# Performance work log

Measured on AMD Instinct MI355X. Metric: run time of the kernel, lower is better.

The kernel has to match this reference:

```python
import jax, jax.numpy as jnp
import numpy as np

B, Q, C = 2, 1568, 768
H = 12
FN, S = 8, 196


def setup_inputs() -> dict:
    key = jax.random.key(0)
    ks = jax.random.split(key, 8)
    init = lambda k, shape: jax.random.normal(k, shape, jnp.float32) * 0.02
    return {
        "query": jax.random.normal(ks[0], (B, Q, C), jnp.float32),
        "memory": jax.random.normal(ks[1], (B, FN * S, C), jnp.float32),
        "Wq": init(ks[2], (C, C)),
        "Wkv": init(ks[3], (C, 2 * C)),
        "Wpq": init(ks[4], (C, C)),
        "Wpkv": init(ks[5], (C, 2 * C)),
        "Wproj": init(ks[6], (C, C)),
        "bproj": jnp.zeros((C,), jnp.float32),
        "seq_len": S,
        "num_frames": FN,
    }


def reference(query, memory, Wq, Wkv, Wpq, Wpkv, Wproj, bproj, seq_len, num_frames):
    Bn, N, Cn = memory.shape
    h = H
    d = Cn // h
    Fn, Sn = num_frames, seq_len
    Qn = query.shape[1]
    scale = d ** -0.5

    # stage 1: per-frame spatial attention
    q = query @ Wq                                   # [B,Q,C]
    k, v = jnp.split(memory @ Wkv, 2, axis=-1)       # [B,N,C] each
    qh = q.reshape(Bn, Qn, h, d)
    kh = k.reshape(Bn, Fn, Sn, h, d)
    vh = v.reshape(Bn, Fn, Sn, h, d)
    space_attn = scale * jnp.einsum('bqhd,bfshd->bhqfs', qh, kh)  # [B,h,Q,F,S]
    attn = jax.nn.softmax(space_attn, axis=-1)        # softmax over tokens within each frame
    # per-frame summaries: [B,Q,F,C]
    x = jnp.einsum('bhqfs,bfshd->bqfhd', attn, vh).reshape(Bn, Qn, Fn, Cn)

    # stage 2: temporal attention over frame summaries
    k2, v2 = jnp.split(x @ Wpkv, 2, axis=-1)
    k2 = k2.reshape(Bn, Qn, Fn, h, d).transpose(0, 3, 1, 2, 4)   # [B,h,Q,F,d]
    v2 = v2.reshape(Bn, Qn, Fn, h, d).transpose(0, 3, 1, 2, 4)   # [B,h,Q,F,d]
    q2 = (q @ Wpq).reshape(Bn, Qn, h, d).transpose(0, 2, 1, 3) * scale  # [B,h,Q,d]
    attn2 = jax.nn.softmax(jnp.einsum('bhqd,bhqfd->bhqf', q2, k2), axis=-1)
    # faithful to source einsum 'b h q f, b h s f d -> b h q d': v2's query axis is summed out
    q_out = jnp.einsum('bhqf,bhsfd->bhqd', attn2, v2)             # [B,h,Q,d]
    q_out = q_out.transpose(0, 2, 1, 3).reshape(Bn, Qn, Cn) @ Wproj + bproj

    # source returns pre-softmax scaled scores with shape (B*h, Q, F, S)
    return q_out, space_attn.reshape(Bn * h, Qn, Fn, Sn)
```

## Files before the change

kernel.cpp:

```cpp
#include <hip/hip_runtime.h>

#define B_   2
#define Q_   1568
#define C_   768
#define C2_  1536
#define H_   12
#define D_   64
#define F_   8
#define S_   196
#define N_   1568
constexpr float SCALE = 0.125f;

typedef __bf16 bf16_t;
typedef __bf16 bf16x8 __attribute__((ext_vector_type(8)));
typedef __bf16 bf16x4 __attribute__((ext_vector_type(4)));
typedef float  f32x4  __attribute__((ext_vector_type(4)));

#define AS_G __attribute__((address_space(1)))
#define AS_L __attribute__((address_space(3)))

__device__ inline void load_lds16(const void* g, void* l) {
    __builtin_amdgcn_global_load_lds((const AS_G unsigned int*)g,
                                     (AS_L unsigned int*)l, 16, 0, 0);
}

__global__ __launch_bounds__(256) void cvt_bf16(
    const float* __restrict__ in, bf16_t* __restrict__ out, int n4)
{
    int i = blockIdx.x * 256 + threadIdx.x;
    if (i < n4) {
        float4 v = ((const float4*)in)[i];
        bf16x4 o = { (bf16_t)v.x, (bf16_t)v.y, (bf16_t)v.z, (bf16_t)v.w };
        ((bf16x4*)out)[i] = o;
    }
}

__global__ __launch_bounds__(256) void transpose_cvt(
    const float* __restrict__ W, bf16_t* __restrict__ Wt, int K, int N)
{
    __shared__ float tile[32][33];
    const int k0 = blockIdx.y * 32, n0 = blockIdx.x * 32;
    const int t = threadIdx.x;
    const int tx = t & 31, ty = t >> 5;
#pragma unroll
    for (int i = 0; i < 4; i++)
        tile[ty + i * 8][tx] = W[(size_t)(k0 + ty + i * 8) * N + n0 + tx];
    __syncthreads();
#pragma unroll
    for (int i = 0; i < 4; i++)
        Wt[(size_t)(n0 + ty + i * 8) * K + k0 + tx] = (bf16_t)tile[tx][ty + i * 8];
}

__global__ __launch_bounds__(256) void gemm_mfma(
    const bf16_t* __restrict__ A, const bf16_t* __restrict__ Bt,
    float* __restrict__ C, bf16_t* __restrict__ Cbf,
    int M, int N, int K, const float* __restrict__ bias)
{
    __shared__ bf16_t As[2][128 * 32];
    __shared__ bf16_t Bs[2][128 * 32];
    const int n0 = blockIdx.x * 128;
    const int m0 = blockIdx.y * 128;
    const int t = threadIdx.x;
    const int lane = t & 63;
    const int wv = t >> 6;
    const int wm = wv >> 1, wn = wv & 1;
    const int lane15 = lane & 15, quad = lane >> 4;

    f32x4 acc[4][4];
#pragma unroll
    for (int i = 0; i < 4; i++)
#pragma unroll
        for (int j = 0; j < 4; j++) acc[i][j] = (f32x4){0.f, 0.f, 0.f, 0.f};

    const int row0 = t >> 2,          kc0 = t & 3;
    const int row1 = (256 + t) >> 2,  kc1 = t & 3;
    int rg0 = m0 + row0; if (rg0 >= M) rg0 = M - 1;
    int rg1 = m0 + row1; if (rg1 >= M) rg1 = M - 1;
    const bf16_t* a0 = A  + (size_t)rg0 * K + kc0 * 8;
    const bf16_t* a1 = A  + (size_t)rg1 * K + kc1 * 8;
    const bf16_t* b0 = Bt + (size_t)(n0 + row0) * K + kc0 * 8;
    const bf16_t* b1 = Bt + (size_t)(n0 + row1) * K + kc1 * 8;
    const int dst0 = (0 * 256 + wv * 64) * 16;
    const int dst1 = (1 * 256 + wv * 64) * 16;

    auto stage = [&](int buf, int k0) {
        load_lds16(a0 + k0, (char*)As[buf] + dst0);
        load_lds16(b0 + k0, (char*)Bs[buf] + dst0);
        load_lds16(a1 + k0, (char*)As[buf] + dst1);
        load_lds16(b1 + k0, (char*)Bs[buf] + dst1);
    };

    stage(0, 0);
    __syncthreads();
    int cur = 0;
    for (int k0 = 0; k0 < K; k0 += 32) {
        if (k0 + 32 < K) stage(cur ^ 1, k0 + 32);

        const bf16_t* Ab = As[cur];
        const bf16_t* Bb = Bs[cur];
        bf16x8 af[4], bfr[4];
#pragma unroll
        for (int i = 0; i < 4; i++) {
            af[i]  = *(const bf16x8*)(Ab + (wm * 64 + i * 16 + lane15) * 32 + quad * 8);
            bfr[i] = *(const bf16x8*)(Bb + (wn * 64 + i * 16 + lane15) * 32 + quad * 8);
        }
#pragma unroll
        for (int i = 0; i < 4; i++)
#pragma unroll
            for (int j = 0; j < 4; j++)
                acc[i][j] = __builtin_amdgcn_mfma_f32_16x16x32_bf16(af[i], bfr[j], acc[i][j], 0, 0, 0);

        __syncthreads();
        cur ^= 1;
    }

#pragma unroll
    for (int i = 0; i < 4; i++) {
#pragma unroll
        for (int j = 0; j < 4; j++) {
            int col = n0 + wn * 64 + j * 16 + lane15;
            float bb = bias ? bias[col] : 0.f;
#pragma unroll
            for (int r = 0; r < 4; r++) {
                int row = m0 + wm * 64 + i * 16 + quad * 4 + r;
                if (row < M) {
                    float v = acc[i][j][r] + bb;
                    if (C)   C[(size_t)row * N + col] = v;
                    if (Cbf) Cbf[(size_t)row * N + col] = (bf16_t)v;
                }
            }
        }
    }
}

__global__ __launch_bounds__(448, 4) void attn1_fused(
    const bf16_t* __restrict__ qb, const bf16_t* __restrict__ kvb,
    float* __restrict__ out1, bf16_t* __restrict__ x, float* __restrict__ xsum)
{
    __shared__ bf16_t Vt[64 * 232];
    __shared__ bf16_t Ps[7 * 16 * 232];
    const int f = blockIdx.x, qt = blockIdx.y, z = blockIdx.z;
    const int b = z / H_, h = z - b * H_;
    const int t = threadIdx.x;
    const int lane = t & 63, w = t >> 6;
    const int lane15 = lane & 15, quad = lane >> 4;

    const size_t kvBase = ((size_t)b * N_ + (size_t)f * S_) * C2_;

    const int qrow = qt * 112 + w * 16 + lane15;
    const bf16_t* qp = qb + ((size_t)b * Q_ + qrow) * C_ + h * D_ + quad * 8;
    bf16x8 qa0 = *(const bf16x8*)(qp);
    bf16x8 qa1 = *(const bf16x8*)(qp + 32);

#pragma unroll
    for (int i = 0; i < 4; i++) {
        int e = t + 448 * i;
        if (e < 64 * 28) {
            int dd = e / 28;
            int s  = S_ + (e - dd * 28);
            Vt[dd * 232 + s] = (bf16_t)0.f;
        }
    }
#pragma unroll
    for (int i = 0; i < 4; i++) {
        int e = t + 448 * i;
        if (e < 8 * S_) {
            int dg = e / S_, s = e - dg * S_;
            bf16x8 v = *(const bf16x8*)(kvb + kvBase + (size_t)s * C2_ + C_ + h * D_ + dg * 8);
#pragma unroll
            for (int j = 0; j < 8; j++)
                Vt[(dg * 8 + j) * 232 + s] = v[j];
        }
    }
    bf16_t* Pw = Ps + w * (16 * 232);
    {
        int prow = lane >> 2, c0 = 208 + (lane & 3) * 4;
        *(bf16x4*)(Pw + prow * 232 + c0) =
            (bf16x4){(bf16_t)0.f, (bf16_t)0.f, (bf16_t)0.f, (bf16_t)0.f};
    }
    __syncthreads();

    f32x4 acc[13];
#pragma unroll
    for (int n = 0; n < 13; n++) acc[n] = (f32x4){0.f, 0.f, 0.f, 0.f};
#pragma unroll
    for (int n = 0; n < 13; n++) {
        int srow = n * 16 + lane15; if (srow > S_ - 1) srow = S_ - 1;
        const bf16_t* kp = kvb + kvBase + (size_t)srow * C2_ + h * D_ + quad * 8;
        bf16x8 kb0 = *(const bf16x8*)(kp);
        bf16x8 kb1 = *(const bf16x8*)(kp + 32);
        acc[n] = __builtin_amdgcn_mfma_f32_16x16x32_bf16(qa0, kb0, acc[n], 0, 0, 0);
        acc[n] = __builtin_amdgcn_mfma_f32_16x16x32_bf16(qa1, kb1, acc[n], 0, 0, 0);
    }

    const size_t o1base = ((size_t)z * Q_ + qt * 112 + w * 16 + quad * 4) * N_ + (size_t)f * S_;
#pragma unroll
    for (int n = 0; n < 13; n++) {
        int s = n * 16 + lane15;
        bool valid = s < S_;
#pragma unroll
        for (int r = 0; r < 4; r++) {
            float v = SCALE * acc[n][r];
            if (valid) out1[o1base + (size_t)r * N_ + s] = v;
            acc[n][r] = valid ? v : -3e38f;
        }
    }

    float m[4], inv[4];
#pragma unroll
    for (int r = 0; r < 4; r++) {
        float mm = acc[0][r];
#pragma unroll
        for (int n = 1; n < 13; n++) mm = fmaxf(mm, acc[n][r]);
        mm = fmaxf(mm, __shfl_xor(mm, 1));
        mm = fmaxf(mm, __shfl_xor(mm, 2));
        mm = fmaxf(mm, __shfl_xor(mm, 4));
        mm = fmaxf(mm, __shfl_xor(mm, 8));
        m[r] = mm;
    }
#pragma unroll
    for (int r = 0; r < 4; r++) {
        float ss = 0.f;
#pragma unroll
        for (int n = 0; n < 13; n++) {
            float e = __expf(acc[n][r] - m[r]);
            acc[n][r] = e;
            ss += e;
        }
        ss += __shfl_xor(ss, 1);
        ss += __shfl_xor(ss, 2);
        ss += __shfl_xor(ss, 4);
        ss += __shfl_xor(ss, 8);
        inv[r] = 1.f / ss;
    }

#pragma unroll
    for (int n = 0; n < 13; n++)
#pragma unroll
        for (int r = 0; r < 4; r++)
            Pw[(quad * 4 + r) * 232 + n * 16 + lane15] = (bf16_t)(acc[n][r] * inv[r]);

    bf16x8 pa[7];
#pragma unroll
    for (int ks = 0; ks < 7; ks++)
        pa[ks] = *(const bf16x8*)(Pw + lane15 * 232 + ks * 32 + quad * 8);

    f32x4 o[4];
#pragma unroll
    for (int nt = 0; nt < 4; nt++) o[nt] = (f32x4){0.f, 0.f, 0.f, 0.f};
#pragma unroll
    for (int nt = 0; nt < 4; nt++)
#pragma unroll
        for (int ks = 0; ks < 7; ks++) {
            bf16x8 vb = *(const bf16x8*)(Vt + (nt * 16 + lane15) * 232 + ks * 32 + quad * 8);
            o[nt] = __builtin_amdgcn_mfma_f32_16x16x32_bf16(pa[ks], vb, o[nt], 0, 0, 0);
        }

    const int qb2 = qt * 112 + w * 16 + quad * 4;
#pragma unroll
    for (int nt = 0; nt < 4; nt++)
#pragma unroll
        for (int r = 0; r < 4; r++)
            x[(((size_t)(b * Q_ + qb2 + r)) * F_ + f) * C_ + h * D_ + nt * 16 + lane15] =
                (bf16_t)o[nt][r];

    float part[4];
#pragma unroll
    for (int nt = 0; nt < 4; nt++)
        part[nt] = o[nt][0] + o[nt][1] + o[nt][2] + o[nt][3];
    __syncthreads();
    float* red = (float*)Vt;
    if (t < 64) red[t] = 0.f;
    __syncthreads();
#pragma unroll
    for (int nt = 0; nt < 4; nt++)
        atomicAdd(&red[nt * 16 + lane15], part[nt]);
    __syncthreads();
    if (t < 64)
        atomicAdd(&xsum[((size_t)(b * F_ + f)) * C_ + h * D_ + t], red[t]);
}

__global__ __launch_bounds__(256) void vsum_kernel(
    const float* __restrict__ xsum, const float* __restrict__ Wpkv,
    float* __restrict__ vsum)
{
    __shared__ float xs[C_];
    const int bf = blockIdx.x;
    const int t = threadIdx.x;
    for (int i = 0; i < 3; i++) xs[t + 256 * i] = xsum[(size_t)bf * C_ + t + 256 * i];
    __syncthreads();
    for (int i = 0; i < 3; i++) {
        int c2 = t + 256 * i;
        float acc = 0.f;
        for (int c = 0; c < C_; c++) acc += xs[c] * Wpkv[(size_t)c * C2_ + C_ + c2];
        vsum[(size_t)bf * C_ + c2] = acc;
    }
}

__global__ __launch_bounds__(256) void attn2_qout(
    const bf16_t* __restrict__ q2, const bf16_t* __restrict__ k2,
    const float* __restrict__ vsum, bf16_t* __restrict__ qout)
{
    __shared__ float q2s[C_];
    __shared__ float l2s[96];
    __shared__ float p2s[96];
    const int bq = blockIdx.x;
    const int t = threadIdx.x;
    for (int i = 0; i < 3; i++)
        q2s[t + 256 * i] = SCALE * (float)q2[(size_t)bq * C_ + t + 256 * i];
    __syncthreads();

    if (t < 96) {
        int h = t >> 3, fr = t & 7;
        const bf16x8* kr8 = (const bf16x8*)(k2 + ((size_t)bq * F_ + fr) * C_ + h * D_);
        float acc = 0.f;
#pragma unroll
        for (int i = 0; i < 8; i++) {
            bf16x8 kk = kr8[i];
#pragma unroll
            for (int j = 0; j < 8; j++) acc += (float)kk[j] * q2s[h * D_ + i * 8 + j];
        }
        l2s[t] = acc;
    }
    __syncthreads();

    if (t < H_) {
        float mm = -3e38f;
#pragma unroll
        for (int fr = 0; fr < F_; fr++) mm = fmaxf(mm, l2s[t * 8 + fr]);
        float e[F_]; float ss = 0.f;
#pragma unroll
        for (int fr = 0; fr < F_; fr++) { e[fr] = __expf(l2s[t * 8 + fr] - mm); ss += e[fr]; }
        float inv = 1.f / ss;
#pragma unroll
        for (int fr = 0; fr < F_; fr++) p2s[t * 8 + fr] = e[fr] * inv;
    }
    __syncthreads();

    const int b = bq / Q_;
    for (int i = 0; i < 3; i++) {
        int c = t + 256 * i;
        int h = c >> 6;
        float acc = 0.f;
#pragma unroll
        for (int fr = 0; fr < F_; fr++)
            acc += p2s[h * 8 + fr] * vsum[((size_t)(b * F_ + fr)) * C_ + c];
        qout[(size_t)bq * C_ + c] = (bf16_t)acc;
    }
}

extern "C" void kernel_launch(void* const* d_in, const int* in_sizes, int n_in,
                              void* d_out, int out_size, void* d_ws, size_t ws_size,
                              hipStream_t stream) {
    const float* query  = (const float*)d_in[0];
    const float* memory = (const float*)d_in[1];
    const float* Wq     = (const float*)d_in[2];
    const float* Wkv    = (const float*)d_in[3];
    const float* Wpq    = (const float*)d_in[4];
    const float* Wpkv   = (const float*)d_in[5];
    const float* Wproj  = (const float*)d_in[6];
    const float* bproj  = (const float*)d_in[7];

    float* out0 = (float*)d_out;
    float* out1 = (float*)d_out + (size_t)B_ * Q_ * C_;

    char* w = (char*)d_ws;
    bf16_t* kv_bf = (bf16_t*)(w + 0);
    bf16_t* q2b   = (bf16_t*)(w + 28901376);
    bf16_t* k2b   = (bf16_t*)(w + 38535168);
    bf16_t* x_bf  = (bf16_t*)(w + 115605504);
    bf16_t* qry_b = (bf16_t*)(w + 154140672);
    bf16_t* mem_b = (bf16_t*)(w + 158957568);
    bf16_t* q_bf  = (bf16_t*)(w + 163774464);
    bf16_t* qo_bf = (bf16_t*)(w + 168591360);
    bf16_t* Wqt   = (bf16_t*)(w + 173408256);
    bf16_t* Wkvt  = (bf16_t*)(w + 174587904);
    bf16_t* Wpqt  = (bf16_t*)(w + 176947200);
    bf16_t* Wpkvt = (bf16_t*)(w + 178126848);
    bf16_t* Wprjt = (bf16_t*)(w + 180486144);
    float*  xsum  = (float*) (w + 181665792);
    float*  vsum  = (float*) (w + 181714944);

    const int MQ = B_ * Q_;
    const int MN = B_ * N_;
    const int MX = B_ * Q_ * F_;

    cvt_bf16<<<2352, 256, 0, stream>>>(query,  qry_b, MQ * C_ / 4);
    cvt_bf16<<<2352, 256, 0, stream>>>(memory, mem_b, MN * C_ / 4);
    transpose_cvt<<<dim3(24, 24), 256, 0, stream>>>(Wq,    Wqt,   C_, C_);
    transpose_cvt<<<dim3(48, 24), 256, 0, stream>>>(Wkv,   Wkvt,  C_, C2_);
    transpose_cvt<<<dim3(24, 24), 256, 0, stream>>>(Wpq,   Wpqt,  C_, C_);
    transpose_cvt<<<dim3(48, 24), 256, 0, stream>>>(Wpkv,  Wpkvt, C_, C2_);
    transpose_cvt<<<dim3(24, 24), 256, 0, stream>>>(Wproj, Wprjt, C_, C_);

    gemm_mfma<<<dim3(6, 25), 256, 0, stream>>>(qry_b, Wqt, nullptr, q_bf, MQ, C_, C_, nullptr);
    gemm_mfma<<<dim3(12, 25), 256, 0, stream>>>(mem_b, Wkvt, nullptr, kv_bf, MN, C2_, C_, nullptr);
    gemm_mfma<<<dim3(6, 25), 256, 0, stream>>>(q_bf, Wpqt, nullptr, q2b, MQ, C_, C_, nullptr);
    hipMemsetAsync(xsum, 0, (size_t)B_ * F_ * C_ * sizeof(float), stream);
    attn1_fused<<<dim3(F_, 14, B_ * H_), 448, 0, stream>>>(q_bf, kv_bf, out1, x_bf, xsum);
    gemm_mfma<<<dim3(6, 196), 256, 0, stream>>>(x_bf, Wpkvt, nullptr, k2b, MX, C_, C_, nullptr);
    vsum_kernel<<<16, 256, 0, stream>>>(xsum, Wpkv, vsum);
    attn2_qout<<<3136, 256, 0, stream>>>(q2b, k2b, vsum, qo_bf);
    gemm_mfma<<<dim3(6, 25), 256, 0, stream>>>(qo_bf, Wprjt, out0, nullptr, MQ, C_, C_, bproj);
}
```

Baseline: 692.2 us.

## Fuse temporal attention logits into K2 GEMM epilogue, drop k2 materialization

The x@Wpkv GEMM epilogue now takes the dot product of its accumulator tile with the matching q2 slice, reduces across lanes with shuffles, and writes per-head/frame logits directly. The 38MB bf16 k2 buffer is no longer written or re-read. attn2_qout shrinks to a shuffle-based softmax over those logits, and vsum_kernel is spread over three times as many blocks. The epilogue adds an LDS staging step and an extra barrier, and each logit is now summed from bf16-rounded q2 against fp32 accumulators.

```diff
diff --git a/kernel.cpp b/kernel.cpp
--- a/kernel.cpp
+++ b/kernel.cpp
@@ -54,7 +54,8 @@
 __global__ __launch_bounds__(256) void gemm_mfma(
     const bf16_t* __restrict__ A, const bf16_t* __restrict__ Bt,
     float* __restrict__ C, bf16_t* __restrict__ Cbf,
-    int M, int N, int K, const float* __restrict__ bias)
+    int M, int N, int K, const float* __restrict__ bias,
+    const bf16_t* __restrict__ q2e, float* __restrict__ l2out)
 {
     __shared__ bf16_t As[2][128 * 32];
     __shared__ bf16_t Bs[2][128 * 32];
@@ -114,19 +115,54 @@
         cur ^= 1;
     }
 
-#pragma unroll
-    for (int i = 0; i < 4; i++) {
-#pragma unroll
-        for (int j = 0; j < 4; j++) {
-            int col = n0 + wn * 64 + j * 16 + lane15;
-            float bb = bias ? bias[col] : 0.f;
+    if (C || Cbf) {
+#pragma unroll
+        for (int i = 0; i < 4; i++) {
+#pragma unroll
+            for (int j = 0; j < 4; j++) {
+                int col = n0 + wn * 64 + j * 16 + lane15;
+                float bb = bias ? bias[col] : 0.f;
+#pragma unroll
+                for (int r = 0; r < 4; r++) {
+                    int row = m0 + wm * 64 + i * 16 + quad * 4 + r;
+                    if (row < M) {
+                        float v = acc[i][j][r] + bb;
+                        if (C)   C[(size_t)row * N + col] = v;
+                        if (Cbf) Cbf[(size_t)row * N + col] = (bf16_t)v;
+                    }
+                }
+            }
+        }
+    }
+
+    if (l2out) {
+        float* q2s = (float*)As;
+        {
+            int qi = t >> 4, cg = t & 15;
+            int bq = (m0 >> 3) + qi;
+            bf16x8 v = *(const bf16x8*)(q2e + (size_t)bq * C_ + n0 + cg * 8);
+#pragma unroll
+            for (int j = 0; j < 8; j++) q2s[qi * 128 + cg * 8 + j] = (float)v[j];
+        }
+        __syncthreads();
+        const int hh = (n0 >> 6) + wn;
+#pragma unroll
+        for (int i = 0; i < 4; i++) {
 #pragma unroll
             for (int r = 0; r < 4; r++) {
-                int row = m0 + wm * 64 + i * 16 + quad * 4 + r;
-                if (row < M) {
-                    float v = acc[i][j][r] + bb;
-                    if (C)   C[(size_t)row * N + col] = v;
-                    if (Cbf) Cbf[(size_t)row * N + col] = (bf16_t)v;
+                int row = wm * 64 + i * 16 + quad * 4 + r;
+                int qi = row >> 3;
+                float s = 0.f;
+#pragma unroll
+                for (int j = 0; j < 4; j++)
+                    s += acc[i][j][r] * q2s[qi * 128 + wn * 64 + j * 16 + lane15];
+                s += __shfl_xor(s, 1);
+                s += __shfl_xor(s, 2);
+                s += __shfl_xor(s, 4);
+                s += __shfl_xor(s, 8);
+                if (lane15 == 0) {
+                    int grow = m0 + row;
+                    l2out[((size_t)(grow >> 3) * H_ + hh) * F_ + (grow & 7)] = SCALE * s;
                 }
             }
         }
@@ -289,51 +325,33 @@
     const int t = threadIdx.x;
     for (int i = 0; i < 3; i++) xs[t + 256 * i] = xsum[(size_t)bf * C_ + t + 256 * i];
     __syncthreads();
-    for (int i = 0; i < 3; i++) {
-        int c2 = t + 256 * i;
-        float acc = 0.f;
-        for (int c = 0; c < C_; c++) acc += xs[c] * Wpkv[(size_t)c * C2_ + C_ + c2];
-        vsum[(size_t)bf * C_ + c2] = acc;
-    }
+    const int c2 = blockIdx.y * 256 + t;
+    float acc = 0.f;
+#pragma unroll 8
+    for (int c = 0; c < C_; c++) acc += xs[c] * Wpkv[(size_t)c * C2_ + C_ + c2];
+    vsum[(size_t)bf * C_ + c2] = acc;
 }
 
 __global__ __launch_bounds__(256) void attn2_qout(
-    const bf16_t* __restrict__ q2, const bf16_t* __restrict__ k2,
-    const float* __restrict__ vsum, bf16_t* __restrict__ qout)
-{
-    __shared__ float q2s[C_];
-    __shared__ float l2s[96];
+    const float* __restrict__ logits2, const float* __restrict__ vsum,
+    bf16_t* __restrict__ qout)
+{
     __shared__ float p2s[96];
     const int bq = blockIdx.x;
     const int t = threadIdx.x;
-    for (int i = 0; i < 3; i++)
-        q2s[t + 256 * i] = SCALE * (float)q2[(size_t)bq * C_ + t + 256 * i];
-    __syncthreads();
 
     if (t < 96) {
-        int h = t >> 3, fr = t & 7;
-        const bf16x8* kr8 = (const bf16x8*)(k2 + ((size_t)bq * F_ + fr) * C_ + h * D_);
-        float acc = 0.f;
-#pragma unroll
-        for (int i = 0; i < 8; i++) {
-            bf16x8 kk = kr8[i];
-#pragma unroll
-            for (int j = 0; j < 8; j++) acc += (float)kk[j] * q2s[h * D_ + i * 8 + j];
-        }
-        l2s[t] = acc;
-    }
-    __syncthreads();
-
-    if (t < H_) {
-        float mm = -3e38f;
-#pragma unroll
-        for (int fr = 0; fr < F_; fr++) mm = fmaxf(mm, l2s[t * 8 + fr]);
-        float e[F_]; float ss = 0.f;
-#pragma unroll
-        for (int fr = 0; fr < F_; fr++) { e[fr] = __expf(l2s[t * 8 + fr] - mm); ss += e[fr]; }
-        float inv = 1.f / ss;
-#pragma unroll
-        for (int fr = 0; fr < F_; fr++) p2s[t * 8 + fr] = e[fr] * inv;
+        float l = logits2[(size_t)bq * 96 + t];
+        float mm = l;
+        mm = fmaxf(mm, __shfl_xor(mm, 1));
+        mm = fmaxf(mm, __shfl_xor(mm, 2));
+        mm = fmaxf(mm, __shfl_xor(mm, 4));
+        float e = __expf(l - mm);
+        float ss = e;
+        ss += __shfl_xor(ss, 1);
+        ss += __shfl_xor(ss, 2);
+        ss += __shfl_xor(ss, 4);
+        p2s[t] = e / ss;
     }
     __syncthreads();
 
@@ -367,7 +385,7 @@
     char* w = (char*)d_ws;
     bf16_t* kv_bf = (bf16_t*)(w + 0);
     bf16_t* q2b   = (bf16_t*)(w + 28901376);
-    bf16_t* k2b   = (bf16_t*)(w + 38535168);
+    float*  lgt2  = (float*) (w + 38535168);
     bf16_t* x_bf  = (bf16_t*)(w + 115605504);
     bf16_t* qry_b = (bf16_t*)(w + 154140672);
     bf16_t* mem_b = (bf16_t*)(w + 158957568);
@@ -393,13 +411,13 @@
     transpose_cvt<<<dim3(48, 24), 256, 0, stream>>>(Wpkv,  Wpkvt, C_, C2_);
     transpose_cvt<<<dim3(24, 24), 256, 0, stream>>>(Wproj, Wprjt, C_, C_);
 
-    gemm_mfma<<<dim3(6, 25), 256, 0, stream>>>(qry_b, Wqt, nullptr, q_bf, MQ, C_, C_, nullptr);
-    gemm_mfma<<<dim3(12, 25), 256, 0, stream>>>(mem_b, Wkvt, nullptr, kv_bf, MN, C2_, C_, nullptr);
-    gemm_mfma<<<dim3(6, 25), 256, 0, stream>>>(q_bf, Wpqt, nullptr, q2b, MQ, C_, C_, nullptr);
+    gemm_mfma<<<dim3(6, 25), 256, 0, stream>>>(qry_b, Wqt, nullptr, q_bf, MQ, C_, C_, nullptr, nullptr, nullptr);
+    gemm_mfma<<<dim3(12, 25), 256, 0, stream>>>(mem_b, Wkvt, nullptr, kv_bf, MN, C2_, C_, nullptr, nullptr, nullptr);
+    gemm_mfma<<<dim3(6, 25), 256, 0, stream>>>(q_bf, Wpqt, nullptr, q2b, MQ, C_, C_, nullptr, nullptr, nullptr);
     hipMemsetAsync(xsum, 0, (size_t)B_ * F_ * C_ * sizeof(float), stream);
     attn1_fused<<<dim3(F_, 14, B_ * H_), 448, 0, stream>>>(q_bf, kv_bf, out1, x_bf, xsum);
-    gemm_mfma<<<dim3(6, 196), 256, 0, stream>>>(x_bf, Wpkvt, nullptr, k2b, MX, C_, C_, nullptr);
-    vsum_kernel<<<16, 256, 0, stream>>>(xsum, Wpkv, vsum);
-    attn2_qout<<<3136, 256, 0, stream>>>(q2b, k2b, vsum, qo_bf);
-    gemm_mfma<<<dim3(6, 25), 256, 0, stream>>>(qo_bf, Wprjt, out0, nullptr, MQ, C_, C_, bproj);
-}
+    gemm_mfma<<<dim3(6, 196), 256, 0, stream>>>(x_bf, Wpkvt, nullptr, nullptr, MX, C_, C_, nullptr, q2b, lgt2);
+    vsum_kernel<<<dim3(16, 3), 256, 0, stream>>>(xsum, Wpkv, vsum);
+    attn2_qout<<<3136, 256, 0, stream>>>(lgt2, vsum, qo_bf);
+    gemm_mfma<<<dim3(6, 25), 256, 0, stream>>>(qo_bf, Wprjt, out0, nullptr, MQ, C_, C_, bproj, nullptr, nullptr);
+}
```

New measurement: 620.2 us. 10.4% less time.
